# Kernel optimization log

Measured on AMD Instinct MI355X. Metric: run time of the kernel, lower is better.

Reference implementation:

```python
import jax, jax.numpy as jnp
import numpy as np

DIM = 768
HEADS = 12
MLP_DIM = 3072
EPS = 1e-5


def setup_inputs() -> dict:
    key = jax.random.key(0)
    ks = jax.random.split(key, 10)
    s = lambda d: 1.0 / np.sqrt(d)
    return {
        "x": jax.random.normal(ks[0], (8, 1024, DIM), dtype=jnp.float32),
        "ln1_g": jnp.ones((DIM,), jnp.float32),
        "ln1_b": jnp.zeros((DIM,), jnp.float32),
        "w_qkv": jax.random.normal(ks[1], (DIM, 3 * DIM), jnp.float32) * s(DIM),
        "w_out": jax.random.normal(ks[2], (DIM, DIM), jnp.float32) * s(DIM),
        "b_out": jnp.zeros((DIM,), jnp.float32),
        "ln2_g": jnp.ones((DIM,), jnp.float32),
        "ln2_b": jnp.zeros((DIM,), jnp.float32),
        "w1": jax.random.normal(ks[3], (DIM, MLP_DIM), jnp.float32) * s(DIM),
        "b1": jnp.zeros((MLP_DIM,), jnp.float32),
        "w2": jax.random.normal(ks[4], (MLP_DIM, DIM), jnp.float32) * s(MLP_DIM),
        "b2": jnp.zeros((DIM,), jnp.float32),
    }


def _layernorm(x, g, b):
    mu = jnp.mean(x, axis=-1, keepdims=True)
    var = jnp.mean(jnp.square(x - mu), axis=-1, keepdims=True)
    return (x - mu) * jax.lax.rsqrt(var + EPS) * g + b


def _block(x, ln1_g, ln1_b, w_qkv, w_out, b_out, ln2_g, ln2_b, w1, b1, w2, b2):
    B, N, C = x.shape
    H = HEADS
    Dh = C // H
    scale = Dh ** -0.5
    # attention
    h = _layernorm(x, ln1_g, ln1_b)
    qkv = (h @ w_qkv).reshape(B, N, 3, H, Dh)
    q, k, v = qkv[:, :, 0], qkv[:, :, 1], qkv[:, :, 2]  # [B,N,H,Dh]
    attn = jnp.einsum("bnhd,bmhd->bhnm", q, k) * scale
    attn = jax.nn.softmax(attn, axis=-1)
    o = jnp.einsum("bhnm,bmhd->bnhd", attn, v).reshape(B, N, C)
    x = x + o @ w_out + b_out
    # mlp (exact erf GELU, matching torch nn.GELU default)
    h = _layernorm(x, ln2_g, ln2_b)
    h = jax.nn.gelu(h @ w1 + b1, approximate=False)
    x = x + h @ w2 + b2
    return x


def reference(x, ln1_g, ln1_b, w_qkv, w_out, b_out, ln2_g, ln2_b, w1, b1, w2, b2):
    return _block(x, ln1_g, ln1_b, w_qkv, w_out, b_out, ln2_g, ln2_b, w1, b1, w2, b2)
```

## Files before the change

kernel.cpp:

```cpp
#include <hip/hip_runtime.h>
#include <hip/hip_bf16.h>
#include <cstdint>

#define DIM 768
#define HEADS 12
#define DH 64
#define MLP_DIM 3072
#define ROWS 8192
#define SEQ 1024
#define PPAD 72
#define ISTR 136

typedef __attribute__((ext_vector_type(8))) short bf16x8;
typedef __attribute__((ext_vector_type(4))) float f32x4;

typedef __attribute__((address_space(1))) void GV;
typedef __attribute__((address_space(3))) void SV;

__device__ inline void async16(const void* g, void* l) {
  __builtin_amdgcn_global_load_lds((GV*)(void*)g, (SV*)l, 16, 0, 0);
}

__device__ inline unsigned short f2b(float f) {
  union { float f; uint32_t u; } v; v.f = f;
  uint32_t u = v.u;
  return (unsigned short)((u + 0x7fffu + ((u >> 16) & 1u)) >> 16);
}

__device__ inline float gelu_f(float v) {
  float x = v * 0.70710678118654752f;
  float ax = fabsf(x);
  float t = 1.f / (1.f + 0.47047f * ax);
  float poly = t * (0.3480242f + t * (-0.0958798f + t * 0.7478556f));
  float erfv = 1.f - poly * __expf(-ax * ax);
  erfv = copysignf(erfv, x);
  return 0.5f * v * (1.f + erfv);
}

__global__ __launch_bounds__(256) void transpose_k(const float* __restrict__ in,
                                                   unsigned short* __restrict__ out,
                                                   int K, int N) {
  __shared__ float t[32][33];
  int tx = threadIdx.x & 31, ty = threadIdx.x >> 5;
  int bn = blockIdx.x * 32, bk = blockIdx.y * 32;
#pragma unroll
  for (int i = ty; i < 32; i += 8) t[i][tx] = in[(size_t)(bk + i) * N + bn + tx];
  __syncthreads();
#pragma unroll
  for (int i = ty; i < 32; i += 8) out[(size_t)(bn + i) * K + bk + tx] = f2b(t[tx][i]);
}

__global__ __launch_bounds__(256) void ln_k(const float* __restrict__ x,
                                            const float* __restrict__ g,
                                            const float* __restrict__ b,
                                            unsigned short* __restrict__ h) {
  int wave = threadIdx.x >> 6, lane = threadIdx.x & 63;
  int row = blockIdx.x * 4 + wave;
  const float* xr = x + (size_t)row * DIM;
  float v[12];
  float s = 0.f;
#pragma unroll
  for (int j = 0; j < 12; ++j) { v[j] = xr[lane + j * 64]; s += v[j]; }
#pragma unroll
  for (int m = 1; m < 64; m <<= 1) s += __shfl_xor(s, m);
  float mu = s * (1.f / DIM);
  float vs = 0.f;
#pragma unroll
  for (int j = 0; j < 12; ++j) { float d = v[j] - mu; vs += d * d; }
#pragma unroll
  for (int m = 1; m < 64; m <<= 1) vs += __shfl_xor(vs, m);
  float rstd = rsqrtf(vs * (1.f / DIM) + 1e-5f);
  unsigned short* hr = h + (size_t)row * DIM;
#pragma unroll
  for (int j = 0; j < 12; ++j) {
    int i = lane + j * 64;
    hr[i] = f2b((v[j] - mu) * rstd * g[i] + b[i]);
  }
}

template <int MODE, int TM>
__global__ __launch_bounds__(256, 2) void gemm_k(
    const unsigned short* __restrict__ A, const unsigned short* __restrict__ Bt,
    int N, int K,
    const float* __restrict__ bias, const float* __restrict__ resid,
    float* __restrict__ outf, unsigned short* __restrict__ outb,
    unsigned short* __restrict__ Qb, unsigned short* __restrict__ Kb,
    unsigned short* __restrict__ Vt) {
  constexpr int MI = (TM == 128) ? 4 : 2;
  constexpr int ASH = TM * 64;
  constexpr int SMEMS = (TM == 128) ? ((MODE == 2) ? 128 * ISTR : 16384) : 12288;
  __shared__ __align__(16) unsigned short smem[SMEMS];
  int tid = threadIdx.x;
  int wave = tid >> 6, lane = tid & 63, lrow = lane & 15, qd = lane >> 4;
  int ntn = N >> 7;
  int bm = (blockIdx.x / ntn) * TM;
  int bn = (blockIdx.x % ntn) << 7;
  int wm = (TM == 128) ? (wave >> 1) * 64 : (wave & 1) * 32;
  int wn = (TM == 128) ? (wave & 1) * 64 : (wave >> 1) * 64;

  f32x4 acc[MI][4];
#pragma unroll
  for (int i = 0; i < MI; ++i)
#pragma unroll
    for (int j = 0; j < 4; ++j) acc[i][j] = (f32x4){0.f, 0.f, 0.f, 0.f};

  int srow = tid >> 3;
  int c = (tid & 7) ^ (srow & 7);
  const char* gA = (const char*)(A + (size_t)(bm + srow) * K) + c * 16;
  const char* gB = (const char*)(Bt + (size_t)(bn + srow) * K) + c * 16;
  char* lA = (char*)smem + tid * 16;
  char* lB = (char*)smem + ASH * 2 + tid * 16;
  size_t rstep = (size_t)32 * K * 2;

  const unsigned short* As = smem;
  const unsigned short* Bs = smem + ASH;

  uint4 pa0, pa1, pa2, pa3, pb0, pb1, pb2, pb3;
  pa0 = *(const uint4*)(gA);
  pa1 = *(const uint4*)(gA + rstep);
  if constexpr (TM == 128) {
    pa2 = *(const uint4*)(gA + 2 * rstep);
    pa3 = *(const uint4*)(gA + 3 * rstep);
  }
  pb0 = *(const uint4*)(gB);
  pb1 = *(const uint4*)(gB + rstep);
  pb2 = *(const uint4*)(gB + 2 * rstep);
  pb3 = *(const uint4*)(gB + 3 * rstep);

  int nk = K >> 6;
  for (int kt = 0; kt < nk; ++kt) {
    *(uint4*)(lA) = pa0;
    *(uint4*)(lA + 4096) = pa1;
    if constexpr (TM == 128) {
      *(uint4*)(lA + 8192) = pa2;
      *(uint4*)(lA + 12288) = pa3;
    }
    *(uint4*)(lB) = pb0;
    *(uint4*)(lB + 4096) = pb1;
    *(uint4*)(lB + 8192) = pb2;
    *(uint4*)(lB + 12288) = pb3;
    __syncthreads();
    if (kt + 1 < nk) {
      size_t k2 = (size_t)(kt + 1) * 128;
      pa0 = *(const uint4*)(gA + k2);
      pa1 = *(const uint4*)(gA + k2 + rstep);
      if constexpr (TM == 128) {
        pa2 = *(const uint4*)(gA + k2 + 2 * rstep);
        pa3 = *(const uint4*)(gA + k2 + 3 * rstep);
      }
      pb0 = *(const uint4*)(gB + k2);
      pb1 = *(const uint4*)(gB + k2 + rstep);
      pb2 = *(const uint4*)(gB + k2 + 2 * rstep);
      pb3 = *(const uint4*)(gB + k2 + 3 * rstep);
    }
#pragma unroll
    for (int s = 0; s < 2; ++s) {
      int q = s * 4 + qd;
      bf16x8 af[MI], bfr[4];
#pragma unroll
      for (int i = 0; i < MI; ++i) {
        int r = wm + i * 16 + lrow;
        af[i] = *(const bf16x8*)(As + r * 64 + ((q ^ (r & 7)) << 3));
      }
#pragma unroll
      for (int i = 0; i < 4; ++i) {
        int r = wn + i * 16 + lrow;
        bfr[i] = *(const bf16x8*)(Bs + r * 64 + ((q ^ (r & 7)) << 3));
      }
#pragma unroll
      for (int mi = 0; mi < MI; ++mi)
#pragma unroll
        for (int ni = 0; ni < 4; ++ni)
          acc[mi][ni] = __builtin_amdgcn_mfma_f32_16x16x32_bf16(af[mi], bfr[ni], acc[mi][ni], 0, 0, 0);
    }
    __syncthreads();
  }

  if (MODE == 1) {
#pragma unroll
    for (int mi = 0; mi < MI; ++mi)
#pragma unroll
      for (int ni = 0; ni < 4; ++ni)
#pragma unroll
        for (int r = 0; r < 4; ++r) {
          int row = bm + wm + mi * 16 + qd * 4 + r;
          int col = bn + wn + ni * 16 + lrow;
          float v = acc[mi][ni][r] + bias[col] + resid[(size_t)row * 768 + col];
          outf[(size_t)row * 768 + col] = v;
        }
  } else if (MODE == 2) {
    unsigned short* img = smem;
#pragma unroll
    for (int mi = 0; mi < MI; ++mi)
#pragma unroll
      for (int ni = 0; ni < 4; ++ni)
#pragma unroll
        for (int r = 0; r < 4; ++r) {
          int lc = wn + ni * 16 + lrow;
          float v = acc[mi][ni][r] + bias[bn + lc];
          img[(wm + mi * 16 + qd * 4 + r) * ISTR + lc] = f2b(gelu_f(v));
        }
    __syncthreads();
#pragma unroll
    for (int p = 0; p < 2; ++p) {
      int lr = p * 64 + (tid >> 2);
      int cs = (tid & 3) * 32;
      const unsigned short* src = img + lr * ISTR + cs;
      unsigned short* dst = outb + (size_t)(bm + lr) * MLP_DIM + bn + cs;
#pragma unroll
      for (int k = 0; k < 4; ++k) *(uint4*)(dst + k * 8) = *(const uint4*)(src + k * 8);
    }
  } else {
#pragma unroll
    for (int mi = 0; mi < MI; ++mi)
#pragma unroll
      for (int ni = 0; ni < 4; ++ni)
#pragma unroll
        for (int r = 0; r < 4; ++r) {
          int row = bm + wm + mi * 16 + qd * 4 + r;
          int col = bn + wn + ni * 16 + lrow;
          float v = acc[mi][ni][r];
          int which = col / 768;
          int rem = col - which * 768;
          int hh = rem >> 6, dh = rem & 63;
          int bb = row >> 10, n = row & 1023;
          size_t bh = (size_t)(bb * HEADS + hh);
          if (which == 0) {
            Qb[(bh * SEQ + n) * DH + dh] = f2b(v * 0.125f);
          } else if (which == 1) {
            Kb[(bh * SEQ + n) * DH + (((dh >> 3) ^ (n & 7)) << 3) + (dh & 7)] = f2b(v);
          } else {
            Vt[(bh * DH + dh) * SEQ + (n & ~63) +
               ((((n >> 3) & 7) ^ (dh & 7)) << 3) + (n & 7)] = f2b(v);
          }
        }
  }
}

__global__ __launch_bounds__(256, 3) void attn_k(const unsigned short* __restrict__ Qb,
                                                 const unsigned short* __restrict__ Kb,
                                                 const unsigned short* __restrict__ Vt,
                                                 unsigned short* __restrict__ o) {
  __shared__ __align__(16) unsigned short Ks[2][64 * 64];
  __shared__ __align__(16) unsigned short Vs[2][64 * 64];
  __shared__ __align__(16) unsigned short Pa[4][32 * PPAD];
  int tid = threadIdx.x;
  int wave = tid >> 6, lane = tid & 63;
  int lrow = lane & 15, qd = lane >> 4;
  int bh = blockIdx.x % 96;
  int qt = blockIdx.x / 96;
  int b = bh / HEADS, hh = bh % HEADS;
  const unsigned short* Qh = Qb + (size_t)bh * SEQ * DH;
  const char* Kh = (const char*)(Kb + (size_t)bh * SEQ * DH);
  const char* Vh = (const char*)(Vt + (size_t)bh * DH * SEQ);
  int qw = qt * 128 + wave * 32;

  bf16x8 qf[2][2];
#pragma unroll
  for (int qs = 0; qs < 2; ++qs)
#pragma unroll
    for (int hf = 0; hf < 2; ++hf)
      qf[qs][hf] = *(const bf16x8*)(Qh + (qw + qs * 16 + lrow) * DH + hf * 32 + qd * 8);

  f32x4 oacc[2][4];
#pragma unroll
  for (int qs = 0; qs < 2; ++qs)
#pragma unroll
    for (int d = 0; d < 4; ++d) oacc[qs][d] = (f32x4){0.f, 0.f, 0.f, 0.f};
  float li[2] = {0.f, 0.f};
  unsigned short* Pw = Pa[wave];

  auto stage = [&](int t, int buf) {
    const char* kbase = Kh + (size_t)t * 8192;
    char* kd = (char*)Ks[buf];
    async16(kbase + tid * 16, kd + tid * 16);
    async16(kbase + 4096 + tid * 16, kd + 4096 + tid * 16);
    const char* vbase = Vh + (size_t)t * 128;
    char* vd = (char*)Vs[buf];
    async16(vbase + (size_t)(tid >> 3) * 2048 + (tid & 7) * 16, vd + tid * 16);
    async16(vbase + (size_t)((tid >> 3) + 32) * 2048 + (tid & 7) * 16, vd + 4096 + tid * 16);
  };

  stage(0, 0);
  for (int t = 0; t < 16; ++t) {
    asm volatile("s_waitcnt vmcnt(0)" ::: "memory");
    __syncthreads();
    if (t < 15) stage(t + 1, (t + 1) & 1);
    const unsigned short* Kst = Ks[t & 1];
    const unsigned short* Vst = Vs[t & 1];

    f32x4 st[4][2];
#pragma unroll
    for (int kt = 0; kt < 4; ++kt) {
      int krow = kt * 16 + lrow;
      int ksw = krow & 7;
      const unsigned short* Kr = Kst + krow * 64;
      bf16x8 k0 = *(const bf16x8*)(Kr + ((qd ^ ksw) << 3));
      bf16x8 k1 = *(const bf16x8*)(Kr + (((qd + 4) ^ ksw) << 3));
#pragma unroll
      for (int qs = 0; qs < 2; ++qs) {
        f32x4 z = (f32x4){0.f, 0.f, 0.f, 0.f};
        z = __builtin_amdgcn_mfma_f32_16x16x32_bf16(k0, qf[qs][0], z, 0, 0, 0);
        z = __builtin_amdgcn_mfma_f32_16x16x32_bf16(k1, qf[qs][1], z, 0, 0, 0);
        st[kt][qs] = z;
      }
    }

#pragma unroll
    for (int kt = 0; kt < 4; ++kt)
#pragma unroll
      for (int qs = 0; qs < 2; ++qs) {
        float p0 = __expf(st[kt][qs][0]);
        float p1 = __expf(st[kt][qs][1]);
        float p2 = __expf(st[kt][qs][2]);
        float p3 = __expf(st[kt][qs][3]);
        li[qs] += (p0 + p1) + (p2 + p3);
        uint2 pk;
        pk.x = (uint32_t)f2b(p0) | ((uint32_t)f2b(p1) << 16);
        pk.y = (uint32_t)f2b(p2) | ((uint32_t)f2b(p3) << 16);
        *(uint2*)(Pw + (qs * 16 + lrow) * PPAD + kt * 16 + qd * 4) = pk;
      }
    asm volatile("s_waitcnt lgkmcnt(0)" ::: "memory");

    bf16x8 ap[2][2];
#pragma unroll
    for (int qs = 0; qs < 2; ++qs)
#pragma unroll
      for (int kh = 0; kh < 2; ++kh)
        ap[qs][kh] = *(const bf16x8*)(Pw + (qs * 16 + lrow) * PPAD + kh * 32 + qd * 8);

#pragma unroll
    for (int ds = 0; ds < 4; ++ds) {
      int vrow = ds * 16 + lrow;
      int vsw = vrow & 7;
      const unsigned short* Vr = Vst + vrow * 64;
      bf16x8 v0 = *(const bf16x8*)(Vr + ((qd ^ vsw) << 3));
      bf16x8 v1 = *(const bf16x8*)(Vr + (((4 + qd) ^ vsw) << 3));
#pragma unroll
      for (int qs = 0; qs < 2; ++qs) {
        oacc[qs][ds] = __builtin_amdgcn_mfma_f32_16x16x32_bf16(ap[qs][0], v0, oacc[qs][ds], 0, 0, 0);
        oacc[qs][ds] = __builtin_amdgcn_mfma_f32_16x16x32_bf16(ap[qs][1], v1, oacc[qs][ds], 0, 0, 0);
      }
    }
  }

#pragma unroll
  for (int qs = 0; qs < 2; ++qs) {
    li[qs] += __shfl_xor(li[qs], 16);
    li[qs] += __shfl_xor(li[qs], 32);
  }

#pragma unroll
  for (int qs = 0; qs < 2; ++qs)
#pragma unroll
    for (int r = 0; r < 4; ++r) {
      float inv = 1.f / __shfl(li[qs], qd * 4 + r);
      int n = qw + qs * 16 + qd * 4 + r;
#pragma unroll
      for (int ds = 0; ds < 4; ++ds) {
        int dh = ds * 16 + lrow;
        o[((size_t)(b * SEQ + n)) * DIM + hh * DH + dh] = f2b(oacc[qs][ds][r] * inv);
      }
    }
}

extern "C" void kernel_launch(void* const* d_in, const int* in_sizes, int n_in,
                              void* d_out, int out_size, void* d_ws, size_t ws_size,
                              hipStream_t stream) {
  const float* x     = (const float*)d_in[0];
  const float* ln1_g = (const float*)d_in[1];
  const float* ln1_b = (const float*)d_in[2];
  const float* w_qkv = (const float*)d_in[3];
  const float* w_out = (const float*)d_in[4];
  const float* b_out = (const float*)d_in[5];
  const float* ln2_g = (const float*)d_in[6];
  const float* ln2_b = (const float*)d_in[7];
  const float* w1    = (const float*)d_in[8];
  const float* b1    = (const float*)d_in[9];
  const float* w2    = (const float*)d_in[10];
  const float* b2    = (const float*)d_in[11];

  char* ws = (char*)d_ws;
  unsigned short* wqkvT = (unsigned short*)(ws + 0);
  unsigned short* woutT = (unsigned short*)(ws + 3538944);
  unsigned short* w1T   = (unsigned short*)(ws + 4718592);
  unsigned short* w2T   = (unsigned short*)(ws + 9437184);
  float*          x2    = (float*)(ws + 14155776);
  unsigned short* h     = (unsigned short*)(ws + 39321600);
  char* big = ws + 51904512;
  unsigned short* Qb = (unsigned short*)(big);
  unsigned short* Kb = (unsigned short*)(big + 12582912);
  unsigned short* Vt = (unsigned short*)(big + 25165824);
  unsigned short* ob = (unsigned short*)(big + 37748736);
  unsigned short* am = (unsigned short*)(big);

  transpose_k<<<dim3(72, 24), 256, 0, stream>>>(w_qkv, wqkvT, 768, 2304);
  transpose_k<<<dim3(24, 24), 256, 0, stream>>>(w_out, woutT, 768, 768);
  transpose_k<<<dim3(96, 24), 256, 0, stream>>>(w1, w1T, 768, 3072);
  transpose_k<<<dim3(24, 96), 256, 0, stream>>>(w2, w2T, 3072, 768);

  ln_k<<<2048, 256, 0, stream>>>(x, ln1_g, ln1_b, h);
  gemm_k<0, 128><<<64 * 18, 256, 0, stream>>>(h, wqkvT, 2304, 768,
                                              nullptr, nullptr, nullptr, nullptr, Qb, Kb, Vt);
  attn_k<<<768, 256, 0, stream>>>(Qb, Kb, Vt, ob);
  gemm_k<1, 64><<<128 * 6, 256, 0, stream>>>(ob, woutT, 768, 768,
                                             b_out, x, x2, nullptr, nullptr, nullptr, nullptr);
  ln_k<<<2048, 256, 0, stream>>>(x2, ln2_g, ln2_b, h);
  gemm_k<2, 128><<<64 * 24, 256, 0, stream>>>(h, w1T, 3072, 768,
                                              b1, nullptr, nullptr, am, nullptr, nullptr, nullptr);
  gemm_k<1, 64><<<128 * 6, 256, 0, stream>>>(am, w2T, 768, 3072,
                                             b2, x2, (float*)d_out, nullptr, nullptr, nullptr, nullptr);
}
```

Before: 363.3 us.

## Stream GEMM A tiles via async LDS loads, keep B fragments in registers

The GEMM main loop is restructured. A tiles are now double-buffered in shared memory and filled with async global_load_lds, while the B operand is loaded directly from global memory into register fragments, with current and next sets swapped each k-step. Block indices are also remapped so that contiguous row tiles land on the same XCD, which should improve L2 reuse. This removes the register-staged copy of A into LDS and the B tile traffic through LDS, at the cost of more global loads for B per wave and more register pressure.

```diff
diff --git a/kernel.cpp b/kernel.cpp
--- a/kernel.cpp
+++ b/kernel.cpp
@@ -77,6 +77,44 @@
     hr[i] = f2b((v[j] - mu) * rstd * g[i] + b[i]);
   }
 }
+
+
+#define GKSTEP(CUR, NXT, KT)                                              \
+  {                                                                        \
+    asm volatile("s_waitcnt vmcnt(0)" ::: "memory");                       \
+    __syncthreads();                                                       \
+    int kn = (KT) + 1;                                                     \
+    if (kn < nk) {                                                         \
+      const char* ga2 = gA + (size_t)kn * 128;                             \
+      char* ld = (char*)smem + ((kn & 1) ? (ASH * 2) : 0) + tid * 16;      \
+      _Pragma("unroll")                                                    \
+      for (int j = 0; j < TM / 32; ++j)                                    \
+        async16(ga2 + (size_t)j * rstep, ld + j * 4096);                   \
+      const unsigned short* gb2 = gB + (size_t)kn * 64;                    \
+      _Pragma("unroll")                                                    \
+      for (int i = 0; i < 4; ++i) {                                        \
+        NXT[i] = *(const bf16x8*)(gb2 + (size_t)i * bstep);                \
+        NXT[i + 4] = *(const bf16x8*)(gb2 + (size_t)i * bstep + 32);       \
+      }                                                                    \
+    }                                                                      \
+    const unsigned short* Asl = smem + (((KT) & 1) ? ASH : 0);             \
+    _Pragma("unroll")                                                      \
+    for (int s = 0; s < 2; ++s) {                                          \
+      int q = s * 4 + qd;                                                  \
+      bf16x8 af[MI];                                                       \
+      _Pragma("unroll")                                                    \
+      for (int i = 0; i < MI; ++i) {                                       \
+        int r = wm + i * 16 + lrow;                                        \
+        af[i] = *(const bf16x8*)(Asl + r * 64 + ((q ^ (r & 7)) << 3));     \
+      }                                                                    \
+      _Pragma("unroll")                                                    \
+      for (int mi = 0; mi < MI; ++mi)                                      \
+        _Pragma("unroll")                                                  \
+        for (int ni = 0; ni < 4; ++ni)                                     \
+          acc[mi][ni] = __builtin_amdgcn_mfma_f32_16x16x32_bf16(           \
+              af[mi], CUR[s * 4 + ni], acc[mi][ni], 0, 0, 0);              \
+    }                                                                      \
+  }
 
 template <int MODE, int TM>
 __global__ __launch_bounds__(256, 2) void gemm_k(
@@ -88,13 +126,16 @@
     unsigned short* __restrict__ Vt) {
   constexpr int MI = (TM == 128) ? 4 : 2;
   constexpr int ASH = TM * 64;
-  constexpr int SMEMS = (TM == 128) ? ((MODE == 2) ? 128 * ISTR : 16384) : 12288;
+  constexpr int IMGS = (MODE == 2) ? 128 * ISTR : 0;
+  constexpr int SMEMS = (2 * ASH > IMGS) ? 2 * ASH : IMGS;
   __shared__ __align__(16) unsigned short smem[SMEMS];
   int tid = threadIdx.x;
   int wave = tid >> 6, lane = tid & 63, lrow = lane & 15, qd = lane >> 4;
   int ntn = N >> 7;
-  int bm = (blockIdx.x / ntn) * TM;
-  int bn = (blockIdx.x % ntn) << 7;
+  int nm = ROWS / TM;
+  int xcd = blockIdx.x & 7, idx = blockIdx.x >> 3;
+  int bm = (xcd * (nm >> 3) + idx / ntn) * TM;
+  int bn = (idx % ntn) << 7;
   int wm = (TM == 128) ? (wave >> 1) * 64 : (wave & 1) * 32;
   int wn = (TM == 128) ? (wave & 1) * 64 : (wave >> 1) * 64;
 
@@ -107,74 +148,27 @@
   int srow = tid >> 3;
   int c = (tid & 7) ^ (srow & 7);
   const char* gA = (const char*)(A + (size_t)(bm + srow) * K) + c * 16;
-  const char* gB = (const char*)(Bt + (size_t)(bn + srow) * K) + c * 16;
-  char* lA = (char*)smem + tid * 16;
-  char* lB = (char*)smem + ASH * 2 + tid * 16;
   size_t rstep = (size_t)32 * K * 2;
-
-  const unsigned short* As = smem;
-  const unsigned short* Bs = smem + ASH;
-
-  uint4 pa0, pa1, pa2, pa3, pb0, pb1, pb2, pb3;
-  pa0 = *(const uint4*)(gA);
-  pa1 = *(const uint4*)(gA + rstep);
-  if constexpr (TM == 128) {
-    pa2 = *(const uint4*)(gA + 2 * rstep);
-    pa3 = *(const uint4*)(gA + 3 * rstep);
-  }
-  pb0 = *(const uint4*)(gB);
-  pb1 = *(const uint4*)(gB + rstep);
-  pb2 = *(const uint4*)(gB + 2 * rstep);
-  pb3 = *(const uint4*)(gB + 3 * rstep);
+  const unsigned short* gB = Bt + (size_t)(bn + wn + lrow) * K + qd * 8;
+  size_t bstep = (size_t)16 * K;
 
   int nk = K >> 6;
-  for (int kt = 0; kt < nk; ++kt) {
-    *(uint4*)(lA) = pa0;
-    *(uint4*)(lA + 4096) = pa1;
-    if constexpr (TM == 128) {
-      *(uint4*)(lA + 8192) = pa2;
-      *(uint4*)(lA + 12288) = pa3;
+  bf16x8 cb[8], nb[8];
+  {
+    char* ld = (char*)smem + tid * 16;
+#pragma unroll
+    for (int j = 0; j < TM / 32; ++j) async16(gA + (size_t)j * rstep, ld + j * 4096);
+#pragma unroll
+    for (int i = 0; i < 4; ++i) {
+      cb[i] = *(const bf16x8*)(gB + (size_t)i * bstep);
+      cb[i + 4] = *(const bf16x8*)(gB + (size_t)i * bstep + 32);
     }
-    *(uint4*)(lB) = pb0;
-    *(uint4*)(lB + 4096) = pb1;
-    *(uint4*)(lB + 8192) = pb2;
-    *(uint4*)(lB + 12288) = pb3;
-    __syncthreads();
-    if (kt + 1 < nk) {
-      size_t k2 = (size_t)(kt + 1) * 128;
-      pa0 = *(const uint4*)(gA + k2);
-      pa1 = *(const uint4*)(gA + k2 + rstep);
-      if constexpr (TM == 128) {
-        pa2 = *(const uint4*)(gA + k2 + 2 * rstep);
-        pa3 = *(const uint4*)(gA + k2 + 3 * rstep);
-      }
-      pb0 = *(const uint4*)(gB + k2);
-      pb1 = *(const uint4*)(gB + k2 + rstep);
-      pb2 = *(const uint4*)(gB + k2 + 2 * rstep);
-      pb3 = *(const uint4*)(gB + k2 + 3 * rstep);
-    }
-#pragma unroll
-    for (int s = 0; s < 2; ++s) {
-      int q = s * 4 + qd;
-      bf16x8 af[MI], bfr[4];
-#pragma unroll
-      for (int i = 0; i < MI; ++i) {
-        int r = wm + i * 16 + lrow;
-        af[i] = *(const bf16x8*)(As + r * 64 + ((q ^ (r & 7)) << 3));
-      }
-#pragma unroll
-      for (int i = 0; i < 4; ++i) {
-        int r = wn + i * 16 + lrow;
-        bfr[i] = *(const bf16x8*)(Bs + r * 64 + ((q ^ (r & 7)) << 3));
-      }
-#pragma unroll
-      for (int mi = 0; mi < MI; ++mi)
-#pragma unroll
-        for (int ni = 0; ni < 4; ++ni)
-          acc[mi][ni] = __builtin_amdgcn_mfma_f32_16x16x32_bf16(af[mi], bfr[ni], acc[mi][ni], 0, 0, 0);
-    }
-    __syncthreads();
-  }
+  }
+  for (int kt = 0; kt < nk; kt += 2) {
+    GKSTEP(cb, nb, kt);
+    GKSTEP(nb, cb, kt + 1);
+  }
+  __syncthreads();
 
   if (MODE == 1) {
 #pragma unroll
```

Measured after the change: 541.5 us. +49.1%, slower.
